# Kernel tuning notes

Measured on AMD Instinct MI355X. Metric: run time of the kernel, lower is better.

## Reference

```python
import jax, jax.numpy as jnp
import numpy as np

Z, Y, X = 200, 8, 200
XM, YM, ZM = 80.0, 6.0, 80.0  # x_meter, y_meter, z_meter
IMG_H, IMG_W = 256, 512
FEAT_C, OUT_CH = 64, 128
EPS = 1e-8


def create_grid3d():
    # matches torch create_grid3d flattening order (z, y, x), x/y shifted by -0.5
    zz, yy, xx = jnp.meshgrid(jnp.linspace(0.0, 1.0, Z),
                              jnp.linspace(0.0, 1.0, Y),
                              jnp.linspace(0.0, 1.0, X), indexing='ij')
    xyz = jnp.stack([xx.ravel() - 0.5, yy.ravel() - 0.5, zz.ravel()], axis=1)  # (N,3)
    return xyz * jnp.array([XM, YM, ZM], dtype=jnp.float32)


def setup_inputs() -> dict:
    key = jax.random.key(0)
    k1, k2, k3 = jax.random.split(key, 3)
    B = 2
    img_feat = jax.random.normal(k1, (B, FEAT_C, 32, 64), dtype=jnp.float32)
    # realistic pinhole intrinsics so many voxels project in-bounds
    K = jnp.array([[300.0, 0.0, IMG_W / 2.0],
                   [0.0, 300.0, IMG_H / 2.0],
                   [0.0, 0.0, 1.0]], dtype=jnp.float32)
    pix_T_cam = jnp.tile(K[None], (B, 1, 1))
    conv_w = jax.random.normal(k2, (OUT_CH, FEAT_C * Y), dtype=jnp.float32) * 0.02
    conv_b = jax.random.normal(k3, (OUT_CH,), dtype=jnp.float32) * 0.02
    return {"img_feat": img_feat, "pix_T_cam": pix_T_cam, "conv_w": conv_w, "conv_b": conv_b}


def reference(img_feat, pix_T_cam, conv_w, conv_b):
    B, C, H, W = img_feat.shape
    xyz = create_grid3d()  # (N,3), N = Z*Y*X
    pix = jnp.einsum('bij,nj->bni', pix_T_cam, xyz)  # (B,N,3)
    d = pix[..., 2]
    u01 = pix[..., 0] / (d + EPS) / IMG_W  # normalized [0,1] u
    v01 = pix[..., 1] / (d + EPS) / IMG_H
    valid = (u01 >= 0) & (v01 >= 0) & (u01 <= 1) & (v01 <= 1)  # (B,N)

    # grid_sample, align_corners=False, padding_mode='zeros' (D=1 collapses to bilinear)
    gx = u01 * 2.0 - 1.0
    gy = v01 * 2.0 - 1.0
    xp = ((gx + 1.0) * W - 1.0) * 0.5
    yp = ((gy + 1.0) * H - 1.0) * 0.5
    x0f = jnp.floor(xp); y0f = jnp.floor(yp)
    wx1 = xp - x0f; wy1 = yp - y0f
    x0 = x0f.astype(jnp.int32); y0 = y0f.astype(jnp.int32)
    bidx = jnp.arange(B)[:, None]

    def gather(xi, yi):
        ok = (xi >= 0) & (xi < W) & (yi >= 0) & (yi < H)
        xc = jnp.clip(xi, 0, W - 1)
        yc = jnp.clip(yi, 0, H - 1)
        vals = img_feat[bidx, :, yc, xc]  # (B,N,C)
        return vals * ok[..., None].astype(img_feat.dtype)

    v00 = gather(x0, y0)
    v01_ = gather(x0 + 1, y0)
    v10 = gather(x0, y0 + 1)
    v11 = gather(x0 + 1, y0 + 1)
    samp = (v00 * ((1 - wx1) * (1 - wy1))[..., None]
            + v01_ * (wx1 * (1 - wy1))[..., None]
            + v10 * ((1 - wx1) * wy1)[..., None]
            + v11 * (wx1 * wy1)[..., None])  # (B,N,C)
    samp = samp * valid[..., None].astype(samp.dtype)

    bev = samp.reshape(B, Z, Y, X, C)
    # rearrange 'b c d h w -> b (c h) d w' with d=Z, h=Y, w=X
    bev = jnp.transpose(bev, (0, 4, 2, 1, 3)).reshape(B, C * Y, Z, X)
    out = jnp.einsum('bczx,oc->bozx', bev, conv_w) + conv_b[None, :, None, None]
    return out
```

## Files before the change

### kernel.cpp

```cpp
#include <hip/hip_runtime.h>


#define NPOS 40000

typedef short bf16x8 __attribute__((ext_vector_type(8)));
typedef float f32x4  __attribute__((ext_vector_type(4)));

__device__ __forceinline__ unsigned rne16(float f) {
    unsigned u = __float_as_uint(f);
    return (u + 0x7fffu + ((u >> 16) & 1u)) >> 16;
}
__device__ __forceinline__ float lo16(unsigned u) { return __uint_as_float(u << 16); }
__device__ __forceinline__ float hi16(unsigned u) { return __uint_as_float(u & 0xffff0000u); }
__device__ __forceinline__ unsigned cvtpk(float lo, float hi) {
    unsigned r;
    asm("v_cvt_pk_bf16_f32 %0, %1, %2" : "=v"(r) : "v"(lo), "v"(hi));
    return r;
}

__global__ __launch_bounds__(256)
void bili_prep(const float* __restrict__ img, const float* __restrict__ convw,
               unsigned short* __restrict__ imgT, unsigned short* __restrict__ Wp)
{
    const int i = blockIdx.x * 256 + threadIdx.x;
    if (blockIdx.x < 1024) {
        const int c = i & 63, x = (i >> 6) & 63, y = (i >> 12) & 31, b = i >> 17;
        imgT[i] = (unsigned short)rne16(img[((b * 64 + c) * 32 + y) * 64 + x]);
    } else {
        const int j = i - 1024 * 256;
        const int k = j & 511, o = j >> 9;
        const int y = k >> 6, c = k & 63;
        Wp[j] = (unsigned short)rne16(convw[o * 512 + c * 8 + y]);
    }
}

__global__ __launch_bounds__(256, 3)
void bili_main(const uint4* __restrict__ imgTq,
               const unsigned short* __restrict__ Wp,
               const float* __restrict__ pixT,
               const float* __restrict__ convb,
               float* __restrict__ out)
{
    __shared__ uint4  Fb[2][1024];
    __shared__ uint2  offsC[512];
    __shared__ float4 wtsL[512];

    const int t   = threadIdx.x;
    const int bx  = blockIdx.x;
    const int b   = (bx >= 625) ? 1 : 0;
    const int n0  = (bx - b * 625) * 64;

    const int wv  = t >> 6;
    const int ln  = t & 63;
    const int l15 = ln & 15;
    const int lg  = ln >> 4;
    const int g   = t >> 3;
    const int li  = t & 7;

    f32x4 acc0[4], acc1[4];
    {
        float bias0[4], bias1[4];
        #pragma unroll
        for (int r = 0; r < 4; ++r) {
            bias0[r] = convb[wv * 32 +      lg * 4 + r];
            bias1[r] = convb[wv * 32 + 16 + lg * 4 + r];
        }
        #pragma unroll
        for (int nt = 0; nt < 4; ++nt)
            #pragma unroll
            for (int r = 0; r < 4; ++r) { acc0[nt][r] = bias0[r]; acc1[nt][r] = bias1[r]; }
    }

    {
        const float* Kb = pixT + b * 9;
        const float K00 = Kb[0], K01 = Kb[1], K02 = Kb[2];
        const float K10 = Kb[3], K11 = Kb[4], K12 = Kb[5];
        const float K20 = Kb[6], K21 = Kb[7], K22 = Kb[8];

        #pragma unroll
        for (int r = 0; r < 2; ++r) {
            const int p    = r * 256 + t;
            const int nloc = p >> 3;
            const int y    = p & 7;
            const int n = n0 + nloc;
            const int z = n / 200;
            const int x = n - z * 200;

            const float pxv = (x * (1.0f / 199.0f) - 0.5f) * 80.0f;
            const float pzv = (z * (1.0f / 199.0f)) * 80.0f;
            const float pyv = (y * (1.0f / 7.0f) - 0.5f) * 6.0f;

            const float p0 = K00 * pxv + K01 * pyv + K02 * pzv;
            const float p1 = K10 * pxv + K11 * pyv + K12 * pzv;
            const float d  = K20 * pxv + K21 * pyv + K22 * pzv;
            const float inv = __builtin_amdgcn_rcpf(d + 1e-8f);
            const float u01 = p0 * inv * (1.0f / 512.0f);
            const float v01 = p1 * inv * (1.0f / 256.0f);
            const float vf = (u01 >= 0.0f && u01 <= 1.0f &&
                              v01 >= 0.0f && v01 <= 1.0f) ? 1.0f : 0.0f;

            float xp = u01 * 64.0f - 0.5f;
            xp = fminf(fmaxf(xp, -2.0f), 66.0f);
            const float x0f = floorf(xp);
            const float wx = xp - x0f;
            const int x0 = (int)x0f, x1i = x0 + 1;
            const float wx0 = (1.0f - wx) * vf * ((x0  >= 0 && x0  < 64) ? 1.0f : 0.0f);
            const float wx1 = wx          * vf * ((x1i >= 0 && x1i < 64) ? 1.0f : 0.0f);
            const int xi0 = min(max(x0, 0), 63);
            const int xi1 = min(max(x1i, 0), 63);

            float yp = v01 * 32.0f - 0.5f;
            yp = fminf(fmaxf(yp, -2.0f), 34.0f);
            const float y0f = floorf(yp);
            const float wy = yp - y0f;
            const int y0 = (int)y0f, y1i = y0 + 1;
            const float wy0 = (1.0f - wy) * ((y0  >= 0 && y0  < 32) ? 1.0f : 0.0f);
            const float wy1 = wy          * ((y1i >= 0 && y1i < 32) ? 1.0f : 0.0f);
            const int yi0 = min(max(y0, 0), 31);
            const int yi1 = min(max(y1i, 0), 31);

            const unsigned o0 = (unsigned)(((yi0 << 6) + xi0) << 3);
            const unsigned o1 = (unsigned)(((yi0 << 6) + xi1) << 3);
            const unsigned o2 = (unsigned)(((yi1 << 6) + xi0) << 3);
            const unsigned o3 = (unsigned)(((yi1 << 6) + xi1) << 3);

            wtsL[p]  = make_float4(wx0 * wy0, wx1 * wy0, wx0 * wy1, wx1 * wy1);
            offsC[p] = make_uint2(o0 | (o1 << 16), o2 | (o3 << 16));
        }
    }

    __syncthreads();

    const uint4*  imgTb = imgTq + b * 16384;
    const bf16x8* ApG   = (const bf16x8*)Wp;
    const bf16x8* Ap0   = ApG + ((wv * 32 +      l15) * 64 + lg);
    const bf16x8* Ap1   = ApG + ((wv * 32 + 16 + l15) * 64 + lg);

    uint4 sbE[8], sbO[8];

    #define ISSUE_H(q, hb, SB)                                                 \
        _Pragma("unroll")                                                      \
        for (int it2 = 0; it2 < 2; ++it2) {                                    \
            const int pp = ((hb) * 2 + it2) * 32 + g;                          \
            const int n_ = pp >> 1, ys = pp & 1;                               \
            const int p_ = n_ * 8 + 2 * (q) + ys;                              \
            const uint2 oc = offsC[p_];                                        \
            SB[it2 * 4 + 0] = imgTb[(oc.x & 0xffffu) + li];                    \
            SB[it2 * 4 + 1] = imgTb[(oc.x >> 16)     + li];                    \
            SB[it2 * 4 + 2] = imgTb[(oc.y & 0xffffu) + li];                    \
            SB[it2 * 4 + 3] = imgTb[(oc.y >> 16)     + li];                    \
        }

    #define PROC_H(q, hb, SB, buf)                                             \
        _Pragma("unroll")                                                      \
        for (int it2 = 0; it2 < 2; ++it2) {                                    \
            const int pp = ((hb) * 2 + it2) * 32 + g;                          \
            const int n_ = pp >> 1, ys = pp & 1;                               \
            const int p_ = n_ * 8 + 2 * (q) + ys;                              \
            const float4 w = wtsL[p_];                                         \
            float2 ac[4];                                                      \
            _Pragma("unroll")                                                  \
            for (int qq = 0; qq < 4; ++qq) ac[qq] = make_float2(0.0f, 0.0f);   \
            _Pragma("unroll")                                                  \
            for (int j = 0; j < 4; ++j) {                                      \
                const uint4 v = SB[it2 * 4 + j];                               \
                const float ww = (j == 0) ? w.x : (j == 1) ? w.y : (j == 2) ? w.z : w.w; \
                ac[0].x = fmaf(ww, lo16(v.x), ac[0].x);                        \
                ac[0].y = fmaf(ww, hi16(v.x), ac[0].y);                        \
                ac[1].x = fmaf(ww, lo16(v.y), ac[1].x);                        \
                ac[1].y = fmaf(ww, hi16(v.y), ac[1].y);                        \
                ac[2].x = fmaf(ww, lo16(v.z), ac[2].x);                        \
                ac[2].y = fmaf(ww, hi16(v.z), ac[2].y);                        \
                ac[3].x = fmaf(ww, lo16(v.w), ac[3].x);                        \
                ac[3].y = fmaf(ww, hi16(v.w), ac[3].y);                        \
            }                                                                  \
            uint4 pk;                                                          \
            pk.x = cvtpk(ac[0].x, ac[0].y);                                    \
            pk.y = cvtpk(ac[1].x, ac[1].y);                                    \
            pk.z = cvtpk(ac[2].x, ac[2].y);                                    \
            pk.w = cvtpk(ac[3].x, ac[3].y);                                    \
            (buf)[n_ * 16 + ((ys * 8 + li) ^ (n_ & 7))] = pk;                  \
        }

    #define MFMA_H(q, hf, buf)                                                 \
        do {                                                                   \
            const bf16x8* Fv = (const bf16x8*)(buf);                           \
            _Pragma("unroll")                                                  \
            for (int k2 = 0; k2 < 2; ++k2) {                                   \
                const int k = (hf) * 2 + k2;                                   \
                const bf16x8 a0_ = Ap0[((q) * 4 + k) * 4];                     \
                const bf16x8 a1_ = Ap1[((q) * 4 + k) * 4];                     \
                _Pragma("unroll")                                              \
                for (int nt = 0; nt < 4; ++nt) {                               \
                    const int nn = nt * 16 + l15;                              \
                    const bf16x8 bv = Fv[nn * 16 + ((k * 4 + lg) ^ (nn & 7))]; \
                    acc0[nt] = __builtin_amdgcn_mfma_f32_16x16x32_bf16(a0_, bv, acc0[nt], 0, 0, 0); \
                    acc1[nt] = __builtin_amdgcn_mfma_f32_16x16x32_bf16(a1_, bv, acc1[nt], 0, 0, 0); \
                }                                                              \
            }                                                                  \
        } while (0)

    ISSUE_H(0, 0, sbE);
    ISSUE_H(0, 1, sbO);
    PROC_H (0, 0, sbE, Fb[0]);
    ISSUE_H(1, 0, sbE);
    PROC_H (0, 1, sbO, Fb[0]);
    __syncthreads();

    ISSUE_H(1, 1, sbO);
    MFMA_H (0, 0, Fb[0]);
    PROC_H (1, 0, sbE, Fb[1]);
    ISSUE_H(2, 0, sbE);
    MFMA_H (0, 1, Fb[0]);
    PROC_H (1, 1, sbO, Fb[1]);
    __syncthreads();

    ISSUE_H(2, 1, sbO);
    MFMA_H (1, 0, Fb[1]);
    PROC_H (2, 0, sbE, Fb[0]);
    ISSUE_H(3, 0, sbE);
    MFMA_H (1, 1, Fb[1]);
    PROC_H (2, 1, sbO, Fb[0]);
    __syncthreads();

    ISSUE_H(3, 1, sbO);
    MFMA_H (2, 0, Fb[0]);
    PROC_H (3, 0, sbE, Fb[1]);
    MFMA_H (2, 1, Fb[0]);
    PROC_H (3, 1, sbO, Fb[1]);
    __syncthreads();

    MFMA_H (3, 0, Fb[1]);
    MFMA_H (3, 1, Fb[1]);

    #undef ISSUE_H
    #undef PROC_H
    #undef MFMA_H

    {
        float* ob = out + (size_t)(b * 128 + wv * 32) * NPOS + n0;
        #pragma unroll
        for (int nt = 0; nt < 4; ++nt) {
            #pragma unroll
            for (int r = 0; r < 4; ++r) {
                ob[(     lg * 4 + r) * NPOS + nt * 16 + l15] = acc0[nt][r];
                ob[(16 + lg * 4 + r) * NPOS + nt * 16 + l15] = acc1[nt][r];
            }
        }
    }
}

extern "C" void kernel_launch(void* const* d_in, const int* in_sizes, int n_in,
                              void* d_out, int out_size, void* d_ws, size_t ws_size,
                              hipStream_t stream) {
    const float* img   = (const float*)d_in[0];
    const float* pixT  = (const float*)d_in[1];
    const float* convw = (const float*)d_in[2];
    const float* convb = (const float*)d_in[3];
    float* out = (float*)d_out;

    unsigned short* imgT = (unsigned short*)d_ws;
    unsigned short* Wp   = imgT + 262144;

    hipLaunchKernelGGL(bili_prep, dim3(1280), dim3(256), 0, stream,
                       img, convw, imgT, Wp);
    hipLaunchKernelGGL(bili_main, dim3(1250), dim3(256), 0, stream,
                       (const uint4*)imgT, Wp, pixT, convb, out);
}
```

Baseline: 43.56 us.

## Precompute bilinear offsets and weights in prep kernel, read from global in main

Moves the per-voxel projection and bilinear offset/weight computation out of the main kernel into extra blocks of the prep kernel, which write them to workspace buffers. The main kernel reads them directly from global memory instead of building them in shared memory. This frees LDS and the initial barrier, so launch bounds go to 4 blocks per CU, and the barriers become a custom lgkmcnt-only wait. The cost is about 15 MB of extra global write-plus-read traffic, and a fallback kernel is kept for when the workspace is too small.

```diff
diff --git a/kernel.cpp b/kernel.cpp
--- a/kernel.cpp
+++ b/kernel.cpp
@@ -17,38 +17,100 @@
     asm("v_cvt_pk_bf16_f32 %0, %1, %2" : "=v"(r) : "v"(lo), "v"(hi));
     return r;
 }
+__device__ __forceinline__ void tile_barrier() {
+    asm volatile("s_waitcnt lgkmcnt(0)" ::: "memory");
+    __builtin_amdgcn_s_barrier();
+    __builtin_amdgcn_sched_barrier(0);
+}
 
 __global__ __launch_bounds__(256)
 void bili_prep(const float* __restrict__ img, const float* __restrict__ convw,
-               unsigned short* __restrict__ imgT, unsigned short* __restrict__ Wp)
+               const float* __restrict__ pixT,
+               unsigned short* __restrict__ imgT, unsigned short* __restrict__ Wp,
+               uint2* __restrict__ offs_g, float4* __restrict__ wts_g)
 {
-    const int i = blockIdx.x * 256 + threadIdx.x;
+    const int t = threadIdx.x;
+    const int i = blockIdx.x * 256 + t;
     if (blockIdx.x < 1024) {
         const int c = i & 63, x = (i >> 6) & 63, y = (i >> 12) & 31, b = i >> 17;
         imgT[i] = (unsigned short)rne16(img[((b * 64 + c) * 32 + y) * 64 + x]);
-    } else {
+    } else if (blockIdx.x < 1280) {
         const int j = i - 1024 * 256;
         const int k = j & 511, o = j >> 9;
         const int y = k >> 6, c = k & 63;
         Wp[j] = (unsigned short)rne16(convw[o * 512 + c * 8 + y]);
-    }
-}
-
-__global__ __launch_bounds__(256, 3)
+    } else {
+        const int j = i - 1280 * 256;
+        const int b = (j >= 320000) ? 1 : 0;
+        const int r = j - b * 320000;
+        const int n = r >> 3;
+        const int y = r & 7;
+        const int z = n / 200;
+        const int x = n - z * 200;
+
+        const float* Kb = pixT + b * 9;
+        const float K00 = Kb[0], K01 = Kb[1], K02 = Kb[2];
+        const float K10 = Kb[3], K11 = Kb[4], K12 = Kb[5];
+        const float K20 = Kb[6], K21 = Kb[7], K22 = Kb[8];
+
+        const float pxv = (x * (1.0f / 199.0f) - 0.5f) * 80.0f;
+        const float pzv = (z * (1.0f / 199.0f)) * 80.0f;
+        const float pyv = (y * (1.0f / 7.0f) - 0.5f) * 6.0f;
+
+        const float p0 = K00 * pxv + K01 * pyv + K02 * pzv;
+        const float p1 = K10 * pxv + K11 * pyv + K12 * pzv;
+        const float d  = K20 * pxv + K21 * pyv + K22 * pzv;
+        const float inv = __builtin_amdgcn_rcpf(d + 1e-8f);
+        const float u01 = p0 * inv * (1.0f / 512.0f);
+        const float v01 = p1 * inv * (1.0f / 256.0f);
+        const float vf = (u01 >= 0.0f && u01 <= 1.0f &&
+                          v01 >= 0.0f && v01 <= 1.0f) ? 1.0f : 0.0f;
+
+        float xp = u01 * 64.0f - 0.5f;
+        xp = fminf(fmaxf(xp, -2.0f), 66.0f);
+        const float x0f = floorf(xp);
+        const float wx = xp - x0f;
+        const int x0 = (int)x0f, x1i = x0 + 1;
+        const float wx0 = (1.0f - wx) * vf * ((x0  >= 0 && x0  < 64) ? 1.0f : 0.0f);
+        const float wx1 = wx          * vf * ((x1i >= 0 && x1i < 64) ? 1.0f : 0.0f);
+        const int xi0 = min(max(x0, 0), 63);
+        const int xi1 = min(max(x1i, 0), 63);
+
+        float yp = v01 * 32.0f - 0.5f;
+        yp = fminf(fmaxf(yp, -2.0f), 34.0f);
+        const float y0f = floorf(yp);
+        const float wy = yp - y0f;
+        const int y0 = (int)y0f, y1i = y0 + 1;
+        const float wy0 = (1.0f - wy) * ((y0  >= 0 && y0  < 32) ? 1.0f : 0.0f);
+        const float wy1 = wy          * ((y1i >= 0 && y1i < 32) ? 1.0f : 0.0f);
+        const int yi0 = min(max(y0, 0), 31);
+        const int yi1 = min(max(y1i, 0), 31);
+
+        const unsigned o0 = (unsigned)(((yi0 << 6) + xi0) << 3);
+        const unsigned o1 = (unsigned)(((yi0 << 6) + xi1) << 3);
+        const unsigned o2 = (unsigned)(((yi1 << 6) + xi0) << 3);
+        const unsigned o3 = (unsigned)(((yi1 << 6) + xi1) << 3);
+
+        offs_g[j] = make_uint2(o0 | (o1 << 16), o2 | (o3 << 16));
+        wts_g[j]  = make_float4(wx0 * wy0, wx1 * wy0, wx0 * wy1, wx1 * wy1);
+    }
+}
+
+__global__ __launch_bounds__(256, 4)
 void bili_main(const uint4* __restrict__ imgTq,
                const unsigned short* __restrict__ Wp,
-               const float* __restrict__ pixT,
+               const uint2* __restrict__ offs_g,
+               const float4* __restrict__ wts_g,
                const float* __restrict__ convb,
                float* __restrict__ out)
 {
-    __shared__ uint4  Fb[2][1024];
-    __shared__ uint2  offsC[512];
-    __shared__ float4 wtsL[512];
+    __shared__ uint4 Fb[2][1024];
 
     const int t   = threadIdx.x;
     const int bx  = blockIdx.x;
     const int b   = (bx >= 625) ? 1 : 0;
     const int n0  = (bx - b * 625) * 64;
+    const int base = b * 320000 + n0 * 8;
 
     const int wv  = t >> 6;
     const int ln  = t & 63;
@@ -71,66 +133,6 @@
             for (int r = 0; r < 4; ++r) { acc0[nt][r] = bias0[r]; acc1[nt][r] = bias1[r]; }
     }
 
-    {
-        const float* Kb = pixT + b * 9;
-        const float K00 = Kb[0], K01 = Kb[1], K02 = Kb[2];
-        const float K10 = Kb[3], K11 = Kb[4], K12 = Kb[5];
-        const float K20 = Kb[6], K21 = Kb[7], K22 = Kb[8];
-
-        #pragma unroll
-        for (int r = 0; r < 2; ++r) {
-            const int p    = r * 256 + t;
-            const int nloc = p >> 3;
-            const int y    = p & 7;
-            const int n = n0 + nloc;
-            const int z = n / 200;
-            const int x = n - z * 200;
-
-            const float pxv = (x * (1.0f / 199.0f) - 0.5f) * 80.0f;
-            const float pzv = (z * (1.0f / 199.0f)) * 80.0f;
-            const float pyv = (y * (1.0f / 7.0f) - 0.5f) * 6.0f;
-
-            const float p0 = K00 * pxv + K01 * pyv + K02 * pzv;
-            const float p1 = K10 * pxv + K11 * pyv + K12 * pzv;
-            const float d  = K20 * pxv + K21 * pyv + K22 * pzv;
-            const float inv = __builtin_amdgcn_rcpf(d + 1e-8f);
-            const float u01 = p0 * inv * (1.0f / 512.0f);
-            const float v01 = p1 * inv * (1.0f / 256.0f);
-            const float vf = (u01 >= 0.0f && u01 <= 1.0f &&
-                              v01 >= 0.0f && v01 <= 1.0f) ? 1.0f : 0.0f;
-
-            float xp = u01 * 64.0f - 0.5f;
-            xp = fminf(fmaxf(xp, -2.0f), 66.0f);
-            const float x0f = floorf(xp);
-            const float wx = xp - x0f;
-            const int x0 = (int)x0f, x1i = x0 + 1;
-            const float wx0 = (1.0f - wx) * vf * ((x0  >= 0 && x0  < 64) ? 1.0f : 0.0f);
-            const float wx1 = wx          * vf * ((x1i >= 0 && x1i < 64) ? 1.0f : 0.0f);
-            const int xi0 = min(max(x0, 0), 63);
-            const int xi1 = min(max(x1i, 0), 63);
-
-            float yp = v01 * 32.0f - 0.5f;
-            yp = fminf(fmaxf(yp, -2.0f), 34.0f);
-            const float y0f = floorf(yp);
-            const float wy = yp - y0f;
-            const int y0 = (int)y0f, y1i = y0 + 1;
-            const float wy0 = (1.0f - wy) * ((y0  >= 0 && y0  < 32) ? 1.0f : 0.0f);
-            const float wy1 = wy          * ((y1i >= 0 && y1i < 32) ? 1.0f : 0.0f);
-            const int yi0 = min(max(y0, 0), 31);
-            const int yi1 = min(max(y1i, 0), 31);
-
-            const unsigned o0 = (unsigned)(((yi0 << 6) + xi0) << 3);
-            const unsigned o1 = (unsigned)(((yi0 << 6) + xi1) << 3);
-            const unsigned o2 = (unsigned)(((yi1 << 6) + xi0) << 3);
-            const unsigned o3 = (unsigned)(((yi1 << 6) + xi1) << 3);
-
-            wtsL[p]  = make_float4(wx0 * wy0, wx1 * wy0, wx0 * wy1, wx1 * wy1);
-            offsC[p] = make_uint2(o0 | (o1 << 16), o2 | (o3 << 16));
-        }
-    }
-
-    __syncthreads();
-
     const uint4*  imgTb = imgTq + b * 16384;
     const bf16x8* ApG   = (const bf16x8*)Wp;
     const bf16x8* Ap0   = ApG + ((wv * 32 +      l15) * 64 + lg);
@@ -144,7 +146,7 @@
             const int pp = ((hb) * 2 + it2) * 32 + g;                          \
             const int n_ = pp >> 1, ys = pp & 1;                               \
             const int p_ = n_ * 8 + 2 * (q) + ys;                              \
-            const uint2 oc = offsC[p_];                                        \
+            const uint2 oc = offs_g[base + p_];                                \
             SB[it2 * 4 + 0] = imgTb[(oc.x & 0xffffu) + li];                    \
             SB[it2 * 4 + 1] = imgTb[(oc.x >> 16)     + li];                    \
             SB[it2 * 4 + 2] = imgTb[(oc.y & 0xffffu) + li];                    \
@@ -157,7 +159,7 @@
             const int pp = ((hb) * 2 + it2) * 32 + g;                          \
             const int n_ = pp >> 1, ys = pp & 1;                               \
             const int p_ = n_ * 8 + 2 * (q) + ys;                              \
-            const float4 w = wtsL[p_];                                         \
+            const float4 w = wts_g[base + p_];                                 \
             float2 ac[4];                                                      \
             _Pragma("unroll")                                                  \
             for (int qq = 0; qq < 4; ++qq) ac[qq] = make_float2(0.0f, 0.0f);   \
@@ -205,6 +207,222 @@
     PROC_H (0, 0, sbE, Fb[0]);
     ISSUE_H(1, 0, sbE);
     PROC_H (0, 1, sbO, Fb[0]);
+    tile_barrier();
+
+    ISSUE_H(1, 1, sbO);
+    MFMA_H (0, 0, Fb[0]);
+    PROC_H (1, 0, sbE, Fb[1]);
+    ISSUE_H(2, 0, sbE);
+    MFMA_H (0, 1, Fb[0]);
+    PROC_H (1, 1, sbO, Fb[1]);
+    tile_barrier();
+
+    ISSUE_H(2, 1, sbO);
+    MFMA_H (1, 0, Fb[1]);
+    PROC_H (2, 0, sbE, Fb[0]);
+    ISSUE_H(3, 0, sbE);
+    MFMA_H (1, 1, Fb[1]);
+    PROC_H (2, 1, sbO, Fb[0]);
+    tile_barrier();
+
+    ISSUE_H(3, 1, sbO);
+    MFMA_H (2, 0, Fb[0]);
+    PROC_H (3, 0, sbE, Fb[1]);
+    MFMA_H (2, 1, Fb[0]);
+    PROC_H (3, 1, sbO, Fb[1]);
+    tile_barrier();
+
+    MFMA_H (3, 0, Fb[1]);
+    MFMA_H (3, 1, Fb[1]);
+
+    #undef ISSUE_H
+    #undef PROC_H
+    #undef MFMA_H
+
+    {
+        float* ob = out + (size_t)(b * 128 + wv * 32) * NPOS + n0;
+        #pragma unroll
+        for (int nt = 0; nt < 4; ++nt) {
+            #pragma unroll
+            for (int r = 0; r < 4; ++r) {
+                ob[(     lg * 4 + r) * NPOS + nt * 16 + l15] = acc0[nt][r];
+                ob[(16 + lg * 4 + r) * NPOS + nt * 16 + l15] = acc1[nt][r];
+            }
+        }
+    }
+}
+
+__global__ __launch_bounds__(256, 3)
+void bili_main_fb(const uint4* __restrict__ imgTq,
+                  const unsigned short* __restrict__ Wp,
+                  const float* __restrict__ pixT,
+                  const float* __restrict__ convb,
+                  float* __restrict__ out)
+{
+    __shared__ uint4  Fb[2][1024];
+    __shared__ uint2  offsC[512];
+    __shared__ float4 wtsL[512];
+
+    const int t   = threadIdx.x;
+    const int bx  = blockIdx.x;
+    const int b   = (bx >= 625) ? 1 : 0;
+    const int n0  = (bx - b * 625) * 64;
+
+    const int wv  = t >> 6;
+    const int ln  = t & 63;
+    const int l15 = ln & 15;
+    const int lg  = ln >> 4;
+    const int g   = t >> 3;
+    const int li  = t & 7;
+
+    f32x4 acc0[4], acc1[4];
+    {
+        float bias0[4], bias1[4];
+        #pragma unroll
+        for (int r = 0; r < 4; ++r) {
+            bias0[r] = convb[wv * 32 +      lg * 4 + r];
+            bias1[r] = convb[wv * 32 + 16 + lg * 4 + r];
+        }
+        #pragma unroll
+        for (int nt = 0; nt < 4; ++nt)
+            #pragma unroll
+            for (int r = 0; r < 4; ++r) { acc0[nt][r] = bias0[r]; acc1[nt][r] = bias1[r]; }
+    }
+
+    {
+        const float* Kb = pixT + b * 9;
+        const float K00 = Kb[0], K01 = Kb[1], K02 = Kb[2];
+        const float K10 = Kb[3], K11 = Kb[4], K12 = Kb[5];
+        const float K20 = Kb[6], K21 = Kb[7], K22 = Kb[8];
+
+        #pragma unroll
+        for (int r = 0; r < 2; ++r) {
+            const int p    = r * 256 + t;
+            const int nloc = p >> 3;
+            const int y    = p & 7;
+            const int n = n0 + nloc;
+            const int z = n / 200;
+            const int x = n - z * 200;
+
+            const float pxv = (x * (1.0f / 199.0f) - 0.5f) * 80.0f;
+            const float pzv = (z * (1.0f / 199.0f)) * 80.0f;
+            const float pyv = (y * (1.0f / 7.0f) - 0.5f) * 6.0f;
+
+            const float p0 = K00 * pxv + K01 * pyv + K02 * pzv;
+            const float p1 = K10 * pxv + K11 * pyv + K12 * pzv;
+            const float d  = K20 * pxv + K21 * pyv + K22 * pzv;
+            const float inv = __builtin_amdgcn_rcpf(d + 1e-8f);
+            const float u01 = p0 * inv * (1.0f / 512.0f);
+            const float v01 = p1 * inv * (1.0f / 256.0f);
+            const float vf = (u01 >= 0.0f && u01 <= 1.0f &&
+                              v01 >= 0.0f && v01 <= 1.0f) ? 1.0f : 0.0f;
+
+            float xp = u01 * 64.0f - 0.5f;
+            xp = fminf(fmaxf(xp, -2.0f), 66.0f);
+            const float x0f = floorf(xp);
+            const float wx = xp - x0f;
+            const int x0 = (int)x0f, x1i = x0 + 1;
+            const float wx0 = (1.0f - wx) * vf * ((x0  >= 0 && x0  < 64) ? 1.0f : 0.0f);
+            const float wx1 = wx          * vf * ((x1i >= 0 && x1i < 64) ? 1.0f : 0.0f);
+            const int xi0 = min(max(x0, 0), 63);
+            const int xi1 = min(max(x1i, 0), 63);
+
+            float yp = v01 * 32.0f - 0.5f;
+            yp = fminf(fmaxf(yp, -2.0f), 34.0f);
+            const float y0f = floorf(yp);
+            const float wy = yp - y0f;
+            const int y0 = (int)y0f, y1i = y0 + 1;
+            const float wy0 = (1.0f - wy) * ((y0  >= 0 && y0  < 32) ? 1.0f : 0.0f);
+            const float wy1 = wy          * ((y1i >= 0 && y1i < 32) ? 1.0f : 0.0f);
+            const int yi0 = min(max(y0, 0), 31);
+            const int yi1 = min(max(y1i, 0), 31);
+
+            const unsigned o0 = (unsigned)(((yi0 << 6) + xi0) << 3);
+            const unsigned o1 = (unsigned)(((yi0 << 6) + xi1) << 3);
+            const unsigned o2 = (unsigned)(((yi1 << 6) + xi0) << 3);
+            const unsigned o3 = (unsigned)(((yi1 << 6) + xi1) << 3);
+
+            wtsL[p]  = make_float4(wx0 * wy0, wx1 * wy0, wx0 * wy1, wx1 * wy1);
+            offsC[p] = make_uint2(o0 | (o1 << 16), o2 | (o3 << 16));
+        }
+    }
+
+    __syncthreads();
+
+    const uint4*  imgTb = imgTq + b * 16384;
+    const bf16x8* ApG   = (const bf16x8*)Wp;
+    const bf16x8* Ap0   = ApG + ((wv * 32 +      l15) * 64 + lg);
+    const bf16x8* Ap1   = ApG + ((wv * 32 + 16 + l15) * 64 + lg);
+
+    uint4 sbE[8], sbO[8];
+
+    #define ISSUE_H(q, hb, SB)                                                 \
+        _Pragma("unroll")                                                      \
+        for (int it2 = 0; it2 < 2; ++it2) {                                    \
+            const int pp = ((hb) * 2 + it2) * 32 + g;                          \
+            const int n_ = pp >> 1, ys = pp & 1;                               \
+            const int p_ = n_ * 8 + 2 * (q) + ys;                              \
+            const uint2 oc = offsC[p_];                                        \
+            SB[it2 * 4 + 0] = imgTb[(oc.x & 0xffffu) + li];                    \
+            SB[it2 * 4 + 1] = imgTb[(oc.x >> 16)     + li];                    \
+            SB[it2 * 4 + 2] = imgTb[(oc.y & 0xffffu) + li];                    \
+            SB[it2 * 4 + 3] = imgTb[(oc.y >> 16)     + li];                    \
+        }
+
+    #define PROC_H(q, hb, SB, buf)                                             \
+        _Pragma("unroll")                                                      \
+        for (int it2 = 0; it2 < 2; ++it2) {                                    \
+            const int pp = ((hb) * 2 + it2) * 32 + g;                          \
+            const int n_ = pp >> 1, ys = pp & 1;                               \
+            const int p_ = n_ * 8 + 2 * (q) + ys;                              \
+            const float4 w = wtsL[p_];                                         \
+            float2 ac[4];                                                      \
+            _Pragma("unroll")                                                  \
+            for (int qq = 0; qq < 4; ++qq) ac[qq] = make_float2(0.0f, 0.0f);   \
+            _Pragma("unroll")                                                  \
+            for (int j = 0; j < 4; ++j) {                                      \
+                const uint4 v = SB[it2 * 4 + j];                               \
+                const float ww = (j == 0) ? w.x : (j == 1) ? w.y : (j == 2) ? w.z : w.w; \
+                ac[0].x = fmaf(ww, lo16(v.x), ac[0].x);                        \
+                ac[0].y = fmaf(ww, hi16(v.x), ac[0].y);                        \
+                ac[1].x = fmaf(ww, lo16(v.y), ac[1].x);                        \
+                ac[1].y = fmaf(ww, hi16(v.y), ac[1].y);                        \
+                ac[2].x = fmaf(ww, lo16(v.z), ac[2].x);                        \
+                ac[2].y = fmaf(ww, hi16(v.z), ac[2].y);                        \
+                ac[3].x = fmaf(ww, lo16(v.w), ac[3].x);                        \
+                ac[3].y = fmaf(ww, hi16(v.w), ac[3].y);                        \
+            }                                                                  \
+            uint4 pk;                                                          \
+            pk.x = cvtpk(ac[0].x, ac[0].y);                                    \
+            pk.y = cvtpk(ac[1].x, ac[1].y);                                    \
+            pk.z = cvtpk(ac[2].x, ac[2].y);                                    \
+            pk.w = cvtpk(ac[3].x, ac[3].y);                                    \
+            (buf)[n_ * 16 + ((ys * 8 + li) ^ (n_ & 7))] = pk;                  \
+        }
+
+    #define MFMA_H(q, hf, buf)                                                 \
+        do {                                                                   \
+            const bf16x8* Fv = (const bf16x8*)(buf);                           \
+            _Pragma("unroll")                                                  \
+            for (int k2 = 0; k2 < 2; ++k2) {                                   \
+                const int k = (hf) * 2 + k2;                                   \
+                const bf16x8 a0_ = Ap0[((q) * 4 + k) * 4];                     \
+                const bf16x8 a1_ = Ap1[((q) * 4 + k) * 4];                     \
+                _Pragma("unroll")                                              \
+                for (int nt = 0; nt < 4; ++nt) {                               \
+                    const int nn = nt * 16 + l15;                              \
+                    const bf16x8 bv = Fv[nn * 16 + ((k * 4 + lg) ^ (nn & 7))]; \
+                    acc0[nt] = __builtin_amdgcn_mfma_f32_16x16x32_bf16(a0_, bv, acc0[nt], 0, 0, 0); \
+                    acc1[nt] = __builtin_amdgcn_mfma_f32_16x16x32_bf16(a1_, bv, acc1[nt], 0, 0, 0); \
+                }                                                              \
+            }                                                                  \
+        } while (0)
+
+    ISSUE_H(0, 0, sbE);
+    ISSUE_H(0, 1, sbO);
+    PROC_H (0, 0, sbE, Fb[0]);
+    ISSUE_H(1, 0, sbE);
+    PROC_H (0, 1, sbO, Fb[0]);
     __syncthreads();
 
     ISSUE_H(1, 1, sbO);
@@ -261,9 +479,19 @@
 
     unsigned short* imgT = (unsigned short*)d_ws;
     unsigned short* Wp   = imgT + 262144;
-
-    hipLaunchKernelGGL(bili_prep, dim3(1280), dim3(256), 0, stream,
-                       img, convw, imgT, Wp);
-    hipLaunchKernelGGL(bili_main, dim3(1250), dim3(256), 0, stream,
-                       (const uint4*)imgT, Wp, pixT, convb, out);
-}
+    uint2*  offs_g = (uint2*)((char*)d_ws + 655360);
+    float4* wts_g  = (float4*)((char*)d_ws + 5775360);
+    const size_t need = 5775360 + 10240000;
+
+    if (ws_size >= need) {
+        hipLaunchKernelGGL(bili_prep, dim3(3780), dim3(256), 0, stream,
+                           img, convw, pixT, imgT, Wp, offs_g, wts_g);
+        hipLaunchKernelGGL(bili_main, dim3(1250), dim3(256), 0, stream,
+                           (const uint4*)imgT, Wp, offs_g, wts_g, convb, out);
+    } else {
+        hipLaunchKernelGGL(bili_prep, dim3(1280), dim3(256), 0, stream,
+                           img, convw, pixT, imgT, Wp, offs_g, wts_g);
+        hipLaunchKernelGGL(bili_main_fb, dim3(1250), dim3(256), 0, stream,
+                           (const uint4*)imgT, Wp, pixT, convb, out);
+    }
+}
```

Result: slower. 53.66 us (+23.2%).

## Precompute bilinear offsets/weights in prep kernel; gather directly from global per wave

Applied to the files above, without the earlier changes.

Moves the projection and bilinear offset/weight computation into the prep kernel, which writes them to workspace (about 15 MB) for every sample. The main kernel then runs one 32-column tile per wave, reads the offsets and weights from global memory, gathers the bf16 image features straight from global with no LDS staging, and feeds MFMA with conv weights read from global. The aim is to drop LDS use and barriers from the main kernel. In exchange it adds a large round trip of the precomputed tables through global memory. A fallback path keeps the old kernel when the workspace is too small.

```diff
diff --git a/kernel.cpp b/kernel.cpp
--- a/kernel.cpp
+++ b/kernel.cpp
@@ -20,26 +20,187 @@
 
 __global__ __launch_bounds__(256)
 void bili_prep(const float* __restrict__ img, const float* __restrict__ convw,
-               unsigned short* __restrict__ imgT, unsigned short* __restrict__ Wp)
+               const float* __restrict__ pixT,
+               unsigned short* __restrict__ imgT, unsigned short* __restrict__ Wp,
+               uint2* __restrict__ offs_g, float4* __restrict__ wts_g)
 {
-    const int i = blockIdx.x * 256 + threadIdx.x;
+    const int t = threadIdx.x;
+    const int i = blockIdx.x * 256 + t;
     if (blockIdx.x < 1024) {
         const int c = i & 63, x = (i >> 6) & 63, y = (i >> 12) & 31, b = i >> 17;
         imgT[i] = (unsigned short)rne16(img[((b * 64 + c) * 32 + y) * 64 + x]);
-    } else {
+    } else if (blockIdx.x < 1280) {
         const int j = i - 1024 * 256;
         const int k = j & 511, o = j >> 9;
         const int y = k >> 6, c = k & 63;
         Wp[j] = (unsigned short)rne16(convw[o * 512 + c * 8 + y]);
+    } else {
+        const int j = i - 1280 * 256;
+        const int b = (j >= 320000) ? 1 : 0;
+        const int r = j - b * 320000;
+        const int n = r >> 3;
+        const int y = r & 7;
+        const int z = n / 200;
+        const int x = n - z * 200;
+
+        const float* Kb = pixT + b * 9;
+        const float K00 = Kb[0], K01 = Kb[1], K02 = Kb[2];
+        const float K10 = Kb[3], K11 = Kb[4], K12 = Kb[5];
+        const float K20 = Kb[6], K21 = Kb[7], K22 = Kb[8];
+
+        const float pxv = (x * (1.0f / 199.0f) - 0.5f) * 80.0f;
+        const float pzv = (z * (1.0f / 199.0f)) * 80.0f;
+        const float pyv = (y * (1.0f / 7.0f) - 0.5f) * 6.0f;
+
+        const float p0 = K00 * pxv + K01 * pyv + K02 * pzv;
+        const float p1 = K10 * pxv + K11 * pyv + K12 * pzv;
+        const float d  = K20 * pxv + K21 * pyv + K22 * pzv;
+        const float inv = __builtin_amdgcn_rcpf(d + 1e-8f);
+        const float u01 = p0 * inv * (1.0f / 512.0f);
+        const float v01 = p1 * inv * (1.0f / 256.0f);
+        const float vf = (u01 >= 0.0f && u01 <= 1.0f &&
+                          v01 >= 0.0f && v01 <= 1.0f) ? 1.0f : 0.0f;
+
+        float xp = u01 * 64.0f - 0.5f;
+        xp = fminf(fmaxf(xp, -2.0f), 66.0f);
+        const float x0f = floorf(xp);
+        const float wx = xp - x0f;
+        const int x0 = (int)x0f, x1i = x0 + 1;
+        const float wx0 = (1.0f - wx) * vf * ((x0  >= 0 && x0  < 64) ? 1.0f : 0.0f);
+        const float wx1 = wx          * vf * ((x1i >= 0 && x1i < 64) ? 1.0f : 0.0f);
+        const int xi0 = min(max(x0, 0), 63);
+        const int xi1 = min(max(x1i, 0), 63);
+
+        float yp = v01 * 32.0f - 0.5f;
+        yp = fminf(fmaxf(yp, -2.0f), 34.0f);
+        const float y0f = floorf(yp);
+        const float wy = yp - y0f;
+        const int y0 = (int)y0f, y1i = y0 + 1;
+        const float wy0 = (1.0f - wy) * ((y0  >= 0 && y0  < 32) ? 1.0f : 0.0f);
+        const float wy1 = wy          * ((y1i >= 0 && y1i < 32) ? 1.0f : 0.0f);
+        const int yi0 = min(max(y0, 0), 31);
+        const int yi1 = min(max(y1i, 0), 31);
+
+        const unsigned o0 = (unsigned)(((yi0 << 6) + xi0) << 3);
+        const unsigned o1 = (unsigned)(((yi0 << 6) + xi1) << 3);
+        const unsigned o2 = (unsigned)(((yi1 << 6) + xi0) << 3);
+        const unsigned o3 = (unsigned)(((yi1 << 6) + xi1) << 3);
+
+        offs_g[j] = make_uint2(o0 | (o1 << 16), o2 | (o3 << 16));
+        wts_g[j]  = make_float4(wx0 * wy0, wx1 * wy0, wx0 * wy1, wx1 * wy1);
     }
 }
 
 __global__ __launch_bounds__(256, 3)
 void bili_main(const uint4* __restrict__ imgTq,
                const unsigned short* __restrict__ Wp,
-               const float* __restrict__ pixT,
+               const uint2* __restrict__ offs_g,
+               const float4* __restrict__ wts_g,
                const float* __restrict__ convb,
                float* __restrict__ out)
+{
+    const int t    = threadIdx.x;
+    const int wv   = t >> 6;
+    const int ln   = t & 63;
+    const int l15  = ln & 15;
+    const int lg   = ln >> 4;
+
+    const int tile = blockIdx.x * 4 + wv;
+    const int b    = (tile >= 1250) ? 1 : 0;
+    const int n0   = (tile - b * 1250) * 32;
+    const int base = b * 320000 + n0 * 8;
+
+    const uint4*  imgTb = imgTq + b * 16384;
+    const bf16x8* ApG   = (const bf16x8*)Wp;
+
+    f32x4 acc[2][8];
+    #pragma unroll
+    for (int ot = 0; ot < 8; ++ot) {
+        const float4 bv = *(const float4*)(convb + ot * 16 + lg * 4);
+        #pragma unroll
+        for (int nt = 0; nt < 2; ++nt) {
+            acc[nt][ot][0] = bv.x; acc[nt][ot][1] = bv.y;
+            acc[nt][ot][2] = bv.z; acc[nt][ot][3] = bv.w;
+        }
+    }
+
+    #pragma unroll
+    for (int y = 0; y < 8; ++y) {
+        bf16x8 Bf[2][2];
+        #pragma unroll
+        for (int nt = 0; nt < 2; ++nt) {
+            const int p_ = base + (nt * 16 + l15) * 8 + y;
+            const uint2  oc = offs_g[p_];
+            const float4 w  = wts_g[p_];
+            const int c0 = (int)(oc.x & 0xffffu), c1 = (int)(oc.x >> 16);
+            const int c2 = (int)(oc.y & 0xffffu), c3 = (int)(oc.y >> 16);
+            #pragma unroll
+            for (int hi = 0; hi < 2; ++hi) {
+                const int cb = lg + 4 * hi;
+                const uint4 v0 = imgTb[c0 + cb];
+                const uint4 v1 = imgTb[c1 + cb];
+                const uint4 v2 = imgTb[c2 + cb];
+                const uint4 v3 = imgTb[c3 + cb];
+
+                float2 ac[4];
+                #pragma unroll
+                for (int q = 0; q < 4; ++q) ac[q] = make_float2(0.0f, 0.0f);
+
+                #define ACC_C(V, WW)                                           \
+                    ac[0].x = fmaf(WW, lo16((V).x), ac[0].x);                  \
+                    ac[0].y = fmaf(WW, hi16((V).x), ac[0].y);                  \
+                    ac[1].x = fmaf(WW, lo16((V).y), ac[1].x);                  \
+                    ac[1].y = fmaf(WW, hi16((V).y), ac[1].y);                  \
+                    ac[2].x = fmaf(WW, lo16((V).z), ac[2].x);                  \
+                    ac[2].y = fmaf(WW, hi16((V).z), ac[2].y);                  \
+                    ac[3].x = fmaf(WW, lo16((V).w), ac[3].x);                  \
+                    ac[3].y = fmaf(WW, hi16((V).w), ac[3].y);
+                ACC_C(v0, w.x)
+                ACC_C(v1, w.y)
+                ACC_C(v2, w.z)
+                ACC_C(v3, w.w)
+                #undef ACC_C
+
+                uint4 pk;
+                pk.x = cvtpk(ac[0].x, ac[0].y);
+                pk.y = cvtpk(ac[1].x, ac[1].y);
+                pk.z = cvtpk(ac[2].x, ac[2].y);
+                pk.w = cvtpk(ac[3].x, ac[3].y);
+                Bf[nt][hi] = __builtin_bit_cast(bf16x8, pk);
+            }
+        }
+
+        #pragma unroll
+        for (int hi = 0; hi < 2; ++hi) {
+            const int ks = y * 2 + hi;
+            #pragma unroll
+            for (int ot = 0; ot < 8; ++ot) {
+                const bf16x8 a = ApG[(ot * 16 + l15) * 64 + ks * 4 + lg];
+                acc[0][ot] = __builtin_amdgcn_mfma_f32_16x16x32_bf16(a, Bf[0][hi], acc[0][ot], 0, 0, 0);
+                acc[1][ot] = __builtin_amdgcn_mfma_f32_16x16x32_bf16(a, Bf[1][hi], acc[1][ot], 0, 0, 0);
+            }
+        }
+    }
+
+    float* ob = out + (size_t)(b * 128) * NPOS + n0;
+    #pragma unroll
+    for (int ot = 0; ot < 8; ++ot) {
+        #pragma unroll
+        for (int nt = 0; nt < 2; ++nt) {
+            #pragma unroll
+            for (int r = 0; r < 4; ++r) {
+                ob[(ot * 16 + lg * 4 + r) * NPOS + nt * 16 + l15] = acc[nt][ot][r];
+            }
+        }
+    }
+}
+
+__global__ __launch_bounds__(256, 3)
+void bili_main_fb(const uint4* __restrict__ imgTq,
+                  const unsigned short* __restrict__ Wp,
+                  const float* __restrict__ pixT,
+                  const float* __restrict__ convb,
+                  float* __restrict__ out)
 {
     __shared__ uint4  Fb[2][1024];
     __shared__ uint2  offsC[512];
@@ -261,9 +422,19 @@
 
     unsigned short* imgT = (unsigned short*)d_ws;
     unsigned short* Wp   = imgT + 262144;
-
-    hipLaunchKernelGGL(bili_prep, dim3(1280), dim3(256), 0, stream,
-                       img, convw, imgT, Wp);
-    hipLaunchKernelGGL(bili_main, dim3(1250), dim3(256), 0, stream,
-                       (const uint4*)imgT, Wp, pixT, convb, out);
-}
+    uint2*  offs_g = (uint2*)((char*)d_ws + 655360);
+    float4* wts_g  = (float4*)((char*)d_ws + 5775360);
+    const size_t need = 5775360 + 10240000;
+
+    if (ws_size >= need) {
+        hipLaunchKernelGGL(bili_prep, dim3(3780), dim3(256), 0, stream,
+                           img, convw, pixT, imgT, Wp, offs_g, wts_g);
+        hipLaunchKernelGGL(bili_main, dim3(625), dim3(256), 0, stream,
+                           (const uint4*)imgT, Wp, offs_g, wts_g, convb, out);
+    } else {
+        hipLaunchKernelGGL(bili_prep, dim3(1280), dim3(256), 0, stream,
+                           img, convw, pixT, imgT, Wp, offs_g, wts_g);
+        hipLaunchKernelGGL(bili_main_fb, dim3(1250), dim3(256), 0, stream,
+                           (const uint4*)imgT, Wp, pixT, convb, out);
+    }
+}
```

Result: slower. 90.65 us (+108.1%).
